# Kernel optimization log

Hardware: AMD Instinct MI355X
Metric: run time of the kernel (lower is better)

## Reference

```python
import jax, jax.numpy as jnp
import numpy as np

DIM = 192
HEADS = 6
HSP = 8
WSP = 8
POS_DIM = (DIM // 4) // 4  # 12


def _ln(x, g, b, eps=1e-5):
    m = jnp.mean(x, -1, keepdims=True)
    v = jnp.mean((x - m) ** 2, -1, keepdims=True)
    return (x - m) / jnp.sqrt(v + eps) * g + b


def _rel_tables():
    # rpe_biases: ((2*HSP-1)*(2*WSP-1), 2) float coords of all relative offsets
    bh, bw = np.meshgrid(np.arange(1 - HSP, HSP), np.arange(1 - WSP, WSP), indexing='ij')
    biases = np.stack([bh, bw], -1).reshape(-1, 2).astype(np.float32)
    # relative_position_index: (N, N) int lookup into the bias table
    ch, cw = np.meshgrid(np.arange(HSP), np.arange(WSP), indexing='ij')
    coords = np.stack([ch, cw], 0).reshape(2, -1)  # (2, N)
    rel = coords[:, :, None] - coords[:, None, :]  # (2, N, N)
    idx = (rel[0] + HSP - 1) * (2 * WSP - 1) + (rel[1] + WSP - 1)
    return jnp.asarray(biases), jnp.asarray(idx.astype(np.int32))


def setup_inputs() -> dict:
    key = jax.random.key(0)
    ks = jax.random.split(key, 8)
    B, H, W = 2, 256, 256
    L = H * W
    def lin(k, i, o):
        return jax.random.normal(k, (i, o), jnp.float32) * 0.02
    return {
        'qkv': jax.random.normal(ks[0], (3, B, L, DIM), jnp.float32),
        'w_proj': lin(ks[1], 2, POS_DIM), 'b_proj': jnp.zeros((POS_DIM,), jnp.float32),
        'g1': jnp.ones((POS_DIM,), jnp.float32), 'be1': jnp.zeros((POS_DIM,), jnp.float32),
        'w1': lin(ks[2], POS_DIM, POS_DIM), 'b1': jnp.zeros((POS_DIM,), jnp.float32),
        'g2': jnp.ones((POS_DIM,), jnp.float32), 'be2': jnp.zeros((POS_DIM,), jnp.float32),
        'w2': lin(ks[3], POS_DIM, POS_DIM), 'b2': jnp.zeros((POS_DIM,), jnp.float32),
        'g3': jnp.ones((POS_DIM,), jnp.float32), 'be3': jnp.zeros((POS_DIM,), jnp.float32),
        'w3': lin(ks[4], POS_DIM, HEADS), 'b3': jnp.zeros((HEADS,), jnp.float32),
        'H': H, 'W': W,
    }


def reference(qkv, w_proj, b_proj, g1, be1, w1, b1, g2, be2, w2, b2, g3, be3, w3, b3, H, W):
    B, L, C = qkv.shape[1], qkv.shape[2], qkv.shape[3]
    hd = C // HEADS
    scale = float(hd) ** -0.5
    N = HSP * WSP

    def im2win(x):
        # (B, L, C) -> (B*nW, heads, N, hd)
        x = x.reshape(B, H // HSP, HSP, W // WSP, WSP, C)
        x = x.transpose(0, 1, 3, 2, 4, 5).reshape(-1, N, HEADS, hd)
        return x.transpose(0, 2, 1, 3)

    q = im2win(qkv[0]) * scale
    k = im2win(qkv[1])
    v = im2win(qkv[2])

    attn = jnp.einsum('whnd,whmd->whnm', q, k)  # (B*nW, heads, N, N)

    # dynamic relative position bias via MLP (DynamicPosBias, residual=False)
    biases, rel_idx = _rel_tables()
    p = biases @ w_proj + b_proj
    p = jax.nn.relu(_ln(p, g1, be1)) @ w1 + b1
    p = jax.nn.relu(_ln(p, g2, be2)) @ w2 + b2
    p = jax.nn.relu(_ln(p, g3, be3)) @ w3 + b3  # (n_rel, heads)
    rpb = p[rel_idx.reshape(-1)].reshape(N, N, HEADS).transpose(2, 0, 1)  # (heads, N, N)
    attn = attn + rpb[None]

    attn = jax.nn.softmax(attn, axis=-1)
    x = jnp.einsum('whnm,whmd->whnd', attn, v)  # (B*nW, heads, N, hd)
    x = x.transpose(0, 2, 1, 3).reshape(-1, N, C)

    # windows2img: (B*nW, N, C) -> (B, H, W, C)
    x = x.reshape(B, H // HSP, W // WSP, HSP, WSP, C)
    x = x.transpose(0, 1, 3, 2, 4, 5).reshape(B, H, W, C)
    return x
```

## Files before the change

kernel.cpp:

```cpp
#include <hip/hip_runtime.h>

#define NHEADS 6
#define HD 32
#define CDIM 192
#define NTOK 64
#define NREL 225
#define PDIM 12
#define IMG 256
#define NWW 32
#define NWIN 2048
#define SCALE 0.17677669529663687f

typedef __attribute__((ext_vector_type(8))) short v8s;
typedef __attribute__((ext_vector_type(4))) float v4f;

#define QKS 40
#define VTS 72
#define PTS 72

__device__ __forceinline__ unsigned short f2bf(float f) {
    union { float f; unsigned u; } c; c.f = f;
    unsigned u = c.u + 0x7fffu + ((c.u >> 16) & 1u);
    return (unsigned short)(u >> 16);
}

__device__ __forceinline__ void ln_relu12(const float* x, const float* g,
                                          const float* be, float* y) {
    float m = 0.f;
#pragma unroll
    for (int i = 0; i < PDIM; ++i) m += x[i];
    m *= (1.f / PDIM);
    float v = 0.f;
#pragma unroll
    for (int i = 0; i < PDIM; ++i) { float d = x[i] - m; v += d * d; }
    v *= (1.f / PDIM);
    float inv = rsqrtf(v + 1e-5f);
#pragma unroll
    for (int i = 0; i < PDIM; ++i) {
        float t = (x[i] - m) * inv * g[i] + be[i];
        y[i] = t > 0.f ? t : 0.f;
    }
}

__global__ __launch_bounds__(256) void posbias_kernel(
    const float* __restrict__ wp, const float* __restrict__ bp,
    const float* __restrict__ g1, const float* __restrict__ be1,
    const float* __restrict__ w1, const float* __restrict__ b1,
    const float* __restrict__ g2, const float* __restrict__ be2,
    const float* __restrict__ w2, const float* __restrict__ b2,
    const float* __restrict__ g3, const float* __restrict__ be3,
    const float* __restrict__ w3, const float* __restrict__ b3,
    float* __restrict__ rpb)
{
    __shared__ float p_sh[NREL * NHEADS];
    int r = threadIdx.x;
    if (r < NREL) {
        float x0 = (float)(r / 15 - 7);
        float x1 = (float)(r % 15 - 7);
        float h[PDIM], y[PDIM];
#pragma unroll
        for (int o = 0; o < PDIM; ++o)
            h[o] = x0 * wp[o] + x1 * wp[PDIM + o] + bp[o];
        ln_relu12(h, g1, be1, y);
#pragma unroll
        for (int o = 0; o < PDIM; ++o) {
            float a = b1[o];
#pragma unroll
            for (int i = 0; i < PDIM; ++i) a += y[i] * w1[i * PDIM + o];
            h[o] = a;
        }
        ln_relu12(h, g2, be2, y);
#pragma unroll
        for (int o = 0; o < PDIM; ++o) {
            float a = b2[o];
#pragma unroll
            for (int i = 0; i < PDIM; ++i) a += y[i] * w2[i * PDIM + o];
            h[o] = a;
        }
        ln_relu12(h, g3, be3, y);
#pragma unroll
        for (int o = 0; o < NHEADS; ++o) {
            float a = b3[o];
#pragma unroll
            for (int i = 0; i < PDIM; ++i) a += y[i] * w3[i * NHEADS + o];
            p_sh[r * NHEADS + o] = a;
        }
    }
    __syncthreads();
    int i = blockIdx.x * 256 + threadIdx.x;
    int h = i >> 12;
    int n = (i >> 6) & 63;
    int m = i & 63;
    int idx = ((n >> 3) - (m >> 3) + 7) * 15 + ((n & 7) - (m & 7) + 7);
    rpb[i] = p_sh[idx * NHEADS + h];
}

__global__ __launch_bounds__(256) void win_attn_mfma(
    const float* __restrict__ qkv, const float* __restrict__ rpb,
    float* __restrict__ out)
{
    __shared__ unsigned short qs[NTOK * QKS];
    __shared__ unsigned short ks[NTOK * QKS];
    __shared__ unsigned short vt[HD * VTS];
    __shared__ unsigned short pt[NTOK * PTS];

    const int t = threadIdx.x;
    const int head = blockIdx.x >> 11;
    const int win  = blockIdx.x & (NWIN - 1);
    const int b    = win >> 10;
    const int bh   = (win >> 5) & 31;
    const int bw   = win & 31;

    const int wave = t >> 6;
    const int lane = t & 63;
    const int lw = lane & 15;
    const int lg = lane >> 4;
    const int rowbase = wave * 16;

    float rbias[4][4];
    {
        const float* rpbh = rpb + head * NTOK * NTOK;
#pragma unroll
        for (int ct = 0; ct < 4; ++ct)
#pragma unroll
            for (int r = 0; r < 4; ++r)
                rbias[ct][r] = rpbh[(rowbase + lg * 4 + r) * NTOK + ct * 16 + lw];
    }

    const size_t SST = (size_t)2 * IMG * IMG * CDIM;
    const float* basep = qkv + (size_t)b * IMG * IMG * CDIM;
#pragma unroll
    for (int pass = 0; pass < 2; ++pass) {
        int idx = t + pass * 256;
        int tok = idx >> 3;
        int d   = (idx & 7) * 4;
        size_t loff = ((size_t)(bh * 8 + (tok >> 3)) * IMG + (bw * 8 + (tok & 7))) * CDIM
                    + head * HD + d;
        float4 q4 = *(const float4*)(basep + loff);
        float4 k4 = *(const float4*)(basep + SST + loff);
        float4 v4 = *(const float4*)(basep + 2 * SST + loff);
        *(ushort4*)&qs[tok * QKS + d] = make_ushort4(
            f2bf(q4.x * SCALE), f2bf(q4.y * SCALE), f2bf(q4.z * SCALE), f2bf(q4.w * SCALE));
        *(ushort4*)&ks[tok * QKS + d] = make_ushort4(
            f2bf(k4.x), f2bf(k4.y), f2bf(k4.z), f2bf(k4.w));
        vt[(d + 0) * VTS + tok] = f2bf(v4.x);
        vt[(d + 1) * VTS + tok] = f2bf(v4.y);
        vt[(d + 2) * VTS + tok] = f2bf(v4.z);
        vt[(d + 3) * VTS + tok] = f2bf(v4.w);
    }
    __syncthreads();

    {
        v8s a = *(const v8s*)&qs[(rowbase + lw) * QKS + lg * 8];
        v4f acc[4];
#pragma unroll
        for (int ct = 0; ct < 4; ++ct) {
#pragma unroll
            for (int r = 0; r < 4; ++r) acc[ct][r] = rbias[ct][r];
            v8s bfr = *(const v8s*)&ks[(ct * 16 + lw) * QKS + lg * 8];
            acc[ct] = __builtin_amdgcn_mfma_f32_16x16x32_bf16(a, bfr, acc[ct], 0, 0, 0);
        }
        v4f mx4;
#pragma unroll
        for (int r = 0; r < 4; ++r)
            mx4[r] = fmaxf(fmaxf(acc[0][r], acc[1][r]), fmaxf(acc[2][r], acc[3][r]));
#pragma unroll
        for (int off = 1; off < 16; off <<= 1)
#pragma unroll
            for (int r = 0; r < 4; ++r)
                mx4[r] = fmaxf(mx4[r], __shfl_xor(mx4[r], off));
        v4f s4 = {0.f, 0.f, 0.f, 0.f};
#pragma unroll
        for (int ct = 0; ct < 4; ++ct)
#pragma unroll
            for (int r = 0; r < 4; ++r) {
                acc[ct][r] = __expf(acc[ct][r] - mx4[r]);
                s4[r] += acc[ct][r];
            }
#pragma unroll
        for (int off = 1; off < 16; off <<= 1)
#pragma unroll
            for (int r = 0; r < 4; ++r)
                s4[r] += __shfl_xor(s4[r], off);
        v4f rinv;
#pragma unroll
        for (int r = 0; r < 4; ++r) rinv[r] = 1.f / s4[r];
#pragma unroll
        for (int ct = 0; ct < 4; ++ct)
#pragma unroll
            for (int r = 0; r < 4; ++r)
                pt[(rowbase + lg * 4 + r) * PTS + ct * 16 + lw] =
                    f2bf(acc[ct][r] * rinv[r]);
    }
    __syncthreads();

    {
        v8s pa[2];
#pragma unroll
        for (int kt = 0; kt < 2; ++kt)
            pa[kt] = *(const v8s*)&pt[(rowbase + lw) * PTS + kt * 32 + lg * 8];
        v4f acc2[2] = {};
#pragma unroll
        for (int dt = 0; dt < 2; ++dt)
#pragma unroll
            for (int kt = 0; kt < 2; ++kt) {
                v8s vb = *(const v8s*)&vt[(dt * 16 + lw) * VTS + kt * 32 + lg * 8];
                acc2[dt] = __builtin_amdgcn_mfma_f32_16x16x32_bf16(pa[kt], vb, acc2[dt], 0, 0, 0);
            }
#pragma unroll
        for (int dt = 0; dt < 2; ++dt)
#pragma unroll
            for (int r = 0; r < 4; ++r) {
                int n = rowbase + lg * 4 + r;
                size_t off = (((size_t)b * IMG + bh * 8 + (n >> 3)) * IMG
                              + (bw * 8 + (n & 7))) * CDIM + head * HD + dt * 16 + lw;
                out[off] = acc2[dt][r];
            }
    }
}

extern "C" void kernel_launch(void* const* d_in, const int* in_sizes, int n_in,
                              void* d_out, int out_size, void* d_ws, size_t ws_size,
                              hipStream_t stream) {
    const float* qkv = (const float*)d_in[0];
    const float* wp  = (const float*)d_in[1];
    const float* bp  = (const float*)d_in[2];
    const float* g1  = (const float*)d_in[3];
    const float* be1 = (const float*)d_in[4];
    const float* w1  = (const float*)d_in[5];
    const float* b1  = (const float*)d_in[6];
    const float* g2  = (const float*)d_in[7];
    const float* be2 = (const float*)d_in[8];
    const float* w2  = (const float*)d_in[9];
    const float* b2  = (const float*)d_in[10];
    const float* g3  = (const float*)d_in[11];
    const float* be3 = (const float*)d_in[12];
    const float* w3  = (const float*)d_in[13];
    const float* b3  = (const float*)d_in[14];

    float* rpb = (float*)d_ws;
    posbias_kernel<<<96, 256, 0, stream>>>(wp, bp, g1, be1, w1, b1,
                                           g2, be2, w2, b2, g3, be3, w3, b3, rpb);
    win_attn_mfma<<<NWIN * NHEADS, 256, 0, stream>>>(qkv, rpb, (float*)d_out);
}
```

Measured before the change: 96.75 us.

## Load Q and K fragments directly from global into MFMA registers, drop LDS staging

Q and K are now read straight from global memory into the MFMA operand registers and converted to bf16 there, which removes the qs/ks shared buffers and the barrier after staging. Only V still goes through LDS for the transpose. The launch bound now requests 8 blocks per multiprocessor to raise occupancy, since LDS use drops. K is read redundantly by all four waves, so each K element is loaded four times from global/L2 instead of once, and register pressure may rise.

```diff
diff --git a/kernel.cpp b/kernel.cpp
--- a/kernel.cpp
+++ b/kernel.cpp
@@ -14,7 +14,6 @@
 typedef __attribute__((ext_vector_type(8))) short v8s;
 typedef __attribute__((ext_vector_type(4))) float v4f;
 
-#define QKS 40
 #define VTS 72
 #define PTS 72
 
@@ -95,12 +94,10 @@
     rpb[i] = p_sh[idx * NHEADS + h];
 }
 
-__global__ __launch_bounds__(256) void win_attn_mfma(
+__global__ __launch_bounds__(256, 8) void win_attn_mfma(
     const float* __restrict__ qkv, const float* __restrict__ rpb,
     float* __restrict__ out)
 {
-    __shared__ unsigned short qs[NTOK * QKS];
-    __shared__ unsigned short ks[NTOK * QKS];
     __shared__ unsigned short vt[HD * VTS];
     __shared__ unsigned short pt[NTOK * PTS];
 
@@ -111,55 +108,64 @@
     const int bh   = (win >> 5) & 31;
     const int bw   = win & 31;
 
+    const int lane = t & 63;
     const int wave = t >> 6;
-    const int lane = t & 63;
     const int lw = lane & 15;
     const int lg = lane >> 4;
     const int rowbase = wave * 16;
 
-    float rbias[4][4];
-    {
-        const float* rpbh = rpb + head * NTOK * NTOK;
-#pragma unroll
-        for (int ct = 0; ct < 4; ++ct)
-#pragma unroll
-            for (int r = 0; r < 4; ++r)
-                rbias[ct][r] = rpbh[(rowbase + lg * 4 + r) * NTOK + ct * 16 + lw];
-    }
-
     const size_t SST = (size_t)2 * IMG * IMG * CDIM;
-    const float* basep = qkv + (size_t)b * IMG * IMG * CDIM;
+    const float* basep = qkv + (size_t)b * IMG * IMG * CDIM + head * HD;
+
+    auto toff = [&](int tok) -> size_t {
+        return ((size_t)(bh * 8 + (tok >> 3)) * IMG + (bw * 8 + (tok & 7))) * CDIM;
+    };
+
 #pragma unroll
     for (int pass = 0; pass < 2; ++pass) {
         int idx = t + pass * 256;
         int tok = idx >> 3;
         int d   = (idx & 7) * 4;
-        size_t loff = ((size_t)(bh * 8 + (tok >> 3)) * IMG + (bw * 8 + (tok & 7))) * CDIM
-                    + head * HD + d;
-        float4 q4 = *(const float4*)(basep + loff);
-        float4 k4 = *(const float4*)(basep + SST + loff);
-        float4 v4 = *(const float4*)(basep + 2 * SST + loff);
-        *(ushort4*)&qs[tok * QKS + d] = make_ushort4(
-            f2bf(q4.x * SCALE), f2bf(q4.y * SCALE), f2bf(q4.z * SCALE), f2bf(q4.w * SCALE));
-        *(ushort4*)&ks[tok * QKS + d] = make_ushort4(
-            f2bf(k4.x), f2bf(k4.y), f2bf(k4.z), f2bf(k4.w));
+        float4 v4 = *(const float4*)(basep + 2 * SST + toff(tok) + d);
         vt[(d + 0) * VTS + tok] = f2bf(v4.x);
         vt[(d + 1) * VTS + tok] = f2bf(v4.y);
         vt[(d + 2) * VTS + tok] = f2bf(v4.z);
         vt[(d + 3) * VTS + tok] = f2bf(v4.w);
     }
-    __syncthreads();
-
-    {
-        v8s a = *(const v8s*)&qs[(rowbase + lw) * QKS + lg * 8];
-        v4f acc[4];
+
+    v8s a;
+    {
+        const float* qp = basep + toff(rowbase + lw) + lg * 8;
+        float4 q0 = *(const float4*)qp;
+        float4 q1 = *(const float4*)(qp + 4);
+        a[0] = (short)f2bf(q0.x * SCALE); a[1] = (short)f2bf(q0.y * SCALE);
+        a[2] = (short)f2bf(q0.z * SCALE); a[3] = (short)f2bf(q0.w * SCALE);
+        a[4] = (short)f2bf(q1.x * SCALE); a[5] = (short)f2bf(q1.y * SCALE);
+        a[6] = (short)f2bf(q1.z * SCALE); a[7] = (short)f2bf(q1.w * SCALE);
+    }
+
+    v4f acc[4];
+    {
+        const float* rpbh = rpb + head * NTOK * NTOK
+                          + (rowbase + lg * 4) * NTOK + lw;
 #pragma unroll
         for (int ct = 0; ct < 4; ++ct) {
-#pragma unroll
-            for (int r = 0; r < 4; ++r) acc[ct][r] = rbias[ct][r];
-            v8s bfr = *(const v8s*)&ks[(ct * 16 + lw) * QKS + lg * 8];
+            const float* kp = basep + SST + toff(ct * 16 + lw) + lg * 8;
+            float4 k0 = *(const float4*)kp;
+            float4 k1 = *(const float4*)(kp + 4);
+            v8s bfr;
+            bfr[0] = (short)f2bf(k0.x); bfr[1] = (short)f2bf(k0.y);
+            bfr[2] = (short)f2bf(k0.z); bfr[3] = (short)f2bf(k0.w);
+            bfr[4] = (short)f2bf(k1.x); bfr[5] = (short)f2bf(k1.y);
+            bfr[6] = (short)f2bf(k1.z); bfr[7] = (short)f2bf(k1.w);
+#pragma unroll
+            for (int r = 0; r < 4; ++r)
+                acc[ct][r] = rpbh[r * NTOK + ct * 16];
             acc[ct] = __builtin_amdgcn_mfma_f32_16x16x32_bf16(a, bfr, acc[ct], 0, 0, 0);
         }
+    }
+
+    {
         v4f mx4;
 #pragma unroll
         for (int r = 0; r < 4; ++r)
```

New measurement: 112.5 us. 1.16x slower.
